# Kernel optimization log

Measured on AMD Instinct MI355X. Metric: run time of the kernel, lower is better.

The kernel has to match this reference:

```python
import jax, jax.numpy as jnp
import numpy as np

B, S, D, H = 2, 2048, 1024, 16
DH = D // H
DIM_K = 1024


def setup_inputs() -> dict:
    key = jax.random.key(0)
    ks = jax.random.split(key, 5)
    sc = 0.02
    return {
        "x": jax.random.normal(ks[0], (B, S, D), dtype=jnp.float32),
        "Wq": jax.random.normal(ks[1], (D, DIM_K), dtype=jnp.float32) * sc,
        "Wk": jax.random.normal(ks[2], (D, DIM_K), dtype=jnp.float32) * sc,
        "Wv": jax.random.normal(ks[3], (D, DIM_K), dtype=jnp.float32) * sc,
        "Wo": jax.random.normal(ks[4], (DIM_K, DIM_K), dtype=jnp.float32) * sc,
    }


def reference(x, Wq, Wk, Wv, Wo):
    # projections (Linear, no bias); weights stored as [in, out]
    q = (x @ Wq).reshape(B, S, H, DH).transpose(0, 2, 1, 3)  # [B,H,S,DH]
    k = (x @ Wk).reshape(B, S, H, DH).transpose(0, 2, 1, 3)
    v = (x @ Wv).reshape(B, S, H, DH).transpose(0, 2, 1, 3)

    scores = jnp.einsum("bhqd,bhkd->bhqk", q, k)  # [B,H,S,S]
    # causal mask applied BEFORE scaling, as in the original
    causal_mask = jnp.triu(jnp.ones((S, S), dtype=bool), k=1)
    m_inf = -jnp.finfo(scores.dtype).max
    scores = jnp.where(causal_mask[None, None], m_inf, scores)
    attn = jax.nn.softmax(scores * (DIM_K ** -0.5), axis=-1)

    out = jnp.einsum("bhqk,bhkd->bhqd", attn, v)  # [B,H,S,DH]
    out = out.transpose(0, 2, 1, 3).reshape(B, S, DIM_K)
    return out @ Wo
```

## Files before the change

kernel.cpp:

```cpp
#include <hip/hip_runtime.h>


#define AS1 __attribute__((address_space(1)))
#define AS3 __attribute__((address_space(3)))
#define EXPC2 0.04508422f
#define C24 1.08202128f

typedef __attribute__((ext_vector_type(4))) float f32x4;
typedef __attribute__((ext_vector_type(8))) short bf16x8;

__device__ __forceinline__ void gload16(const void* g, void* l) {
  __builtin_amdgcn_global_load_lds((const AS1 unsigned int*)g,
                                   (AS3 unsigned int*)l, 16, 0, 0);
}
__device__ __forceinline__ unsigned short f2b(float f) {
  unsigned u = __float_as_uint(f);
  return (unsigned short)((u + 0x7FFFu + ((u >> 16) & 1u)) >> 16);
}
__device__ __forceinline__ float fexp2(float x) {
  float r;
  asm("v_exp_f32 %0, %1" : "=v"(r) : "v"(x));
  return r;
}
__device__ __forceinline__ unsigned cvtpk(float a, float b) {
  unsigned r;
  asm("v_cvt_pk_bf16_f32 %0, %1, %2" : "=v"(r) : "v"(a), "v"(b));
  return r;
}

__global__ __launch_bounds__(256) void prep(
    const float* __restrict__ x, const float* __restrict__ W0,
    const float* __restrict__ W1, const float* __restrict__ W2,
    const float* __restrict__ W3, unsigned short* __restrict__ xb,
    unsigned short* __restrict__ Wt) {
  __shared__ float T[64][65];
  const int tid = threadIdx.x;
  const int bid = blockIdx.x;
  if (bid < 4096) {
    const size_t i = (size_t)(bid * 256 + tid) * 4;
    float4 v = *(const float4*)&x[i];
    uint2 o;
    o.x = f2b(v.x) | ((unsigned)f2b(v.y) << 16);
    o.y = f2b(v.z) | ((unsigned)f2b(v.w) << 16);
    *(uint2*)&xb[i] = o;
    return;
  }
  const int idx = bid - 4096;
  const int kb = (idx & 15) * 64, nb = ((idx >> 4) & 15) * 64, z = idx >> 8;
  const float* W = (z == 0) ? W0 : (z == 1) ? W1 : (z == 2) ? W2 : W3;
  unsigned short* D = Wt + (size_t)z * 1024 * 1024;
#pragma unroll
  for (int p = 0; p < 4; ++p) {
    const int s = p * 256 + tid;
    const int r = s >> 4, c4 = s & 15;
    float4 v = *(const float4*)&W[(size_t)(kb + r) * 1024 + nb + c4 * 4];
    T[r][c4 * 4 + 0] = v.x;
    T[r][c4 * 4 + 1] = v.y;
    T[r][c4 * 4 + 2] = v.z;
    T[r][c4 * 4 + 3] = v.w;
  }
  __syncthreads();
#pragma unroll
  for (int p = 0; p < 4; ++p) {
    const int s = p * 256 + tid;
    const int n = s >> 4, k4 = s & 15;
    uint2 o;
    o.x = f2b(T[k4 * 4 + 0][n]) | ((unsigned)f2b(T[k4 * 4 + 1][n]) << 16);
    o.y = f2b(T[k4 * 4 + 2][n]) | ((unsigned)f2b(T[k4 * 4 + 3][n]) << 16);
    *(uint2*)&D[(size_t)(nb + n) * 1024 + kb + k4 * 4] = o;
  }
}

__global__ __launch_bounds__(256) void gemm_qkv(
    const unsigned short* __restrict__ xb, const unsigned short* __restrict__ Wt,
    unsigned short* __restrict__ Qb, unsigned short* __restrict__ Kb,
    unsigned short* __restrict__ Vp) {
  __shared__ unsigned short smem[32768];

  const int tid = threadIdx.x, lane = tid & 63, w = tid >> 6;
  const int bid = blockIdx.x;
  const int xcd = bid & 7, pos = bid >> 3;
  const int sub = pos >> 5, idx = pos & 31;
  const int bm = xcd * 4 + (idx & 3);
  const int bn = sub * 8 + (idx >> 2);
  const int wr = w >> 1, wc = w & 1;

  f32x4 acc[4][4];
#pragma unroll
  for (int m = 0; m < 4; ++m)
#pragma unroll
    for (int n = 0; n < 4; ++n) acc[m][n] = (f32x4)0.0f;

  const int prow0 = tid >> 3, pc0 = tid & 7;
  const int u0 = pc0 ^ (prow0 & 7);
  const int rOff = 2 * prow0 + (u0 >> 2);
  const int cOff = (u0 & 3) * 8;

  const int fr = lane & 15, g = lane >> 4;
  const int frh = fr >> 1;
  const int pcx = ((((fr & 1) << 2) | g) ^ frh) * 8;

#define QST(BUF, KC)                                                          \
  {                                                                           \
    const size_t ko = (size_t)(KC) + cOff;                                    \
    gload16(&xb[(size_t)(bm * 128 + rOff) * 1024 + ko],                       \
            &smem[(BUF)*8192 + tid * 8]);                                     \
    gload16(&xb[(size_t)(bm * 128 + 64 + rOff) * 1024 + ko],                  \
            &smem[(BUF)*8192 + 2048 + tid * 8]);                              \
    gload16(&Wt[(size_t)(bn * 128 + rOff) * 1024 + ko],                       \
            &smem[(BUF)*8192 + 4096 + tid * 8]);                              \
    gload16(&Wt[(size_t)(bn * 128 + 64 + rOff) * 1024 + ko],                  \
            &smem[(BUF)*8192 + 6144 + tid * 8]);                              \
  }

#define QPH(CB, VMSTR, STAGESTMT)                                             \
  {                                                                           \
    asm volatile(VMSTR ::: "memory");                                         \
    __builtin_amdgcn_sched_barrier(0);                                        \
    __builtin_amdgcn_s_barrier();                                             \
    __builtin_amdgcn_sched_barrier(0);                                        \
    bf16x8 af[4], bf[4];                                                      \
    const unsigned short* Ab_ = &smem[(CB)*8192];                             \
    const unsigned short* Bb_ = &smem[(CB)*8192 + 4096];                      \
    _Pragma("unroll") for (int mf = 0; mf < 4; ++mf) af[mf] =                 \
        *(const bf16x8*)&Ab_[(wr * 32 + mf * 8 + frh) * 64 + pcx];            \
    _Pragma("unroll") for (int nf = 0; nf < 4; ++nf) bf[nf] =                 \
        *(const bf16x8*)&Bb_[(wc * 32 + nf * 8 + frh) * 64 + pcx];            \
    STAGESTMT;                                                                \
    __builtin_amdgcn_s_setprio(1);                                            \
    _Pragma("unroll") for (int mf = 0; mf < 4; ++mf)                          \
        _Pragma("unroll") for (int nf = 0; nf < 4; ++nf) acc[mf][nf] =        \
            __builtin_amdgcn_mfma_f32_16x16x32_bf16(af[mf], bf[nf],           \
                                                    acc[mf][nf], 0, 0, 0);    \
    __builtin_amdgcn_s_setprio(0);                                            \
  }

  QST(0, 0)
  QST(1, 32)
  QST(2, 64)

#pragma unroll 1
  for (int t = 0; t < 29; ++t) {
    const int cb = t & 3, sb = (t + 3) & 3, kc = (t + 3) * 32;
    QPH(cb, "s_waitcnt vmcnt(8)", QST(sb, kc))
  }
  QPH(1, "s_waitcnt vmcnt(8)", (void)0)
  QPH(2, "s_waitcnt vmcnt(4)", (void)0)
  QPH(3, "s_waitcnt vmcnt(0)", (void)0)

  if (bn < 16) {
    unsigned short* Ob = (bn < 8) ? Qb : Kb;
    const int cbase = (bn & 7) * 128;
#pragma unroll
    for (int mf = 0; mf < 4; ++mf)
#pragma unroll
      for (int nf = 0; nf < 4; ++nf) {
        const int col = cbase + wc * 64 + nf * 16 + fr;
        const int h = col >> 6, d = col & 63;
#pragma unroll
        for (int rr = 0; rr < 4; ++rr) {
          const int m = bm * 128 + wr * 64 + mf * 16 + g * 4 + rr;
          const int b = m >> 11, s = m & 2047;
          Ob[((size_t)(b * 16 + h) * 2048 + s) * 64 + d] = f2b(acc[mf][nf][rr]);
        }
      }
    return;
  }

  __syncthreads();
#pragma unroll
  for (int mf = 0; mf < 4; ++mf)
#pragma unroll
    for (int nf = 0; nf < 4; ++nf) {
      const int cl = wc * 64 + nf * 16 + fr;
#pragma unroll
      for (int rr = 0; rr < 4; ++rr) {
        const int ml = wr * 64 + mf * 16 + g * 4 + rr;
        const int u = ml & 63, a = u >> 4;
        const int sperm = (ml & 64) | ((a >> 1) * 32 + ((u >> 2) & 3) * 8 +
                                       (a & 1) * 4 + (u & 3));
        smem[cl * 132 + sperm] = f2b(acc[mf][nf][rr]);
      }
    }
  __syncthreads();
  const int l5 = lane & 31;
  const size_t sbase = (size_t)((bm * 128) & 2047);
  const int bV = bm >> 4;
#pragma unroll
  for (int it = 0; it < 16; ++it) {
    const int rl = w * 32 + it * 2 + (lane >> 5);
    const int rowg = (bn - 16) * 128 + rl;
    const int h = rowg >> 6, d = rowg & 63;
    uint2 v = *(const uint2*)&smem[rl * 132 + l5 * 4];
    *(uint2*)&Vp[((size_t)(bV * 16 + h) * 64 + d) * 2048 + sbase + l5 * 4] = v;
  }
#undef QPH
#undef QST
}

__global__ __launch_bounds__(256) void gemm_out(
    const unsigned short* __restrict__ A, const unsigned short* __restrict__ B,
    float* __restrict__ Of) {
  __shared__ unsigned short smem[32768];

  const int tid = threadIdx.x, lane = tid & 63, w = tid >> 6;
  const int bm = blockIdx.x >> 3, bn = blockIdx.x & 7;
  const int wr = w >> 1, wc = w & 1;

  f32x4 acc[4][4];
#pragma unroll
  for (int m = 0; m < 4; ++m)
#pragma unroll
    for (int n = 0; n < 4; ++n) acc[m][n] = (f32x4)0.0f;

  const int prow0 = tid >> 3, pc0 = tid & 7;
  const int u0 = pc0 ^ (prow0 & 7);
  const int rOff = 2 * prow0 + (u0 >> 2);
  const int cOff = (u0 & 3) * 8;

  const int fr = lane & 15, g = lane >> 4;
  const int frh = fr >> 1;
  const int pcx = ((((fr & 1) << 2) | g) ^ frh) * 8;

#define OSTAGE4(BUF, KS, KC)                                                  \
  {                                                                           \
    const size_t ko = (size_t)(KC) + (KS)*32 + cOff;                          \
    gload16(&A[(size_t)(bm * 128 + rOff) * 1024 + ko],                        \
            &smem[(BUF)*16384 + (KS)*4096 + tid * 8]);                        \
    gload16(&A[(size_t)(bm * 128 + 64 + rOff) * 1024 + ko],                   \
            &smem[(BUF)*16384 + (KS)*4096 + 2048 + tid * 8]);                 \
    gload16(&B[(size_t)(bn * 128 + rOff) * 1024 + ko],                        \
            &smem[(BUF)*16384 + 8192 + (KS)*4096 + tid * 8]);                 \
    gload16(&B[(size_t)(bn * 128 + 64 + rOff) * 1024 + ko],                   \
            &smem[(BUF)*16384 + 8192 + (KS)*4096 + 2048 + tid * 8]);          \
  }

#define OPHASE(CUR, KS, VMSTR, STAGESTMT)                                     \
  {                                                                           \
    asm volatile(VMSTR ::: "memory");                                         \
    __builtin_amdgcn_sched_barrier(0);                                        \
    __builtin_amdgcn_s_barrier();                                             \
    __builtin_amdgcn_sched_barrier(0);                                        \
    bf16x8 af[4], bf[4];                                                      \
    const unsigned short* Ab_ = &smem[(CUR)*16384 + (KS)*4096];               \
    const unsigned short* Bb_ = &smem[(CUR)*16384 + 8192 + (KS)*4096];        \
    _Pragma("unroll") for (int mf = 0; mf < 4; ++mf) af[mf] =                 \
        *(const bf16x8*)&Ab_[(wr * 32 + mf * 8 + frh) * 64 + pcx];            \
    _Pragma("unroll") for (int nf = 0; nf < 4; ++nf) bf[nf] =                 \
        *(const bf16x8*)&Bb_[(wc * 32 + nf * 8 + frh) * 64 + pcx];            \
    STAGESTMT;                                                                \
    __builtin_amdgcn_s_setprio(1);                                            \
    _Pragma("unroll") for (int mf = 0; mf < 4; ++mf)                          \
        _Pragma("unroll") for (int nf = 0; nf < 4; ++nf) acc[mf][nf] =        \
            __builtin_amdgcn_mfma_f32_16x16x32_bf16(af[mf], bf[nf],           \
                                                    acc[mf][nf], 0, 0, 0);    \
    __builtin_amdgcn_s_setprio(0);                                            \
  }

  OSTAGE4(0, 0, 0)
  OSTAGE4(0, 1, 0)

#pragma unroll 1
  for (int t = 0; t < 15; ++t) {
    const int cu_ = t & 1, nb_ = (t + 1) & 1;
    const int kc1 = (t + 1) * 64;
    OPHASE(cu_, 0, "s_waitcnt vmcnt(4)", OSTAGE4(nb_, 0, kc1))
    OPHASE(cu_, 1, "s_waitcnt vmcnt(4)", OSTAGE4(nb_, 1, kc1))
  }
  OPHASE(1, 0, "s_waitcnt vmcnt(4)", (void)0)
  OPHASE(1, 1, "s_waitcnt vmcnt(0)", (void)0)

#pragma unroll
  for (int mf = 0; mf < 4; ++mf)
#pragma unroll
    for (int nf = 0; nf < 4; ++nf) {
      const int col = bn * 128 + wc * 64 + nf * 16 + fr;
#pragma unroll
      for (int rr = 0; rr < 4; ++rr) {
        const int m = bm * 128 + wr * 64 + mf * 16 + g * 4 + rr;
        Of[(size_t)m * 1024 + col] = acc[mf][nf][rr];
      }
    }
#undef OPHASE
#undef OSTAGE4
}

__global__ __launch_bounds__(256) void attn_fm(
    const unsigned short* __restrict__ Qb, const unsigned short* __restrict__ Kb,
    const unsigned short* __restrict__ Vp, unsigned short* __restrict__ Ab) {
  __shared__ unsigned short smem[16384];

  const int tid = threadIdx.x, lane = tid & 63, w = tid >> 6;
  const int lo = lane & 15, hi = lane >> 4;

  const int id = blockIdx.x;
  const int bh = (id & 7) * 4 + ((id >> 3) & 3);
  const int rem = id >> 5;
  const int qtr = rem >> 3;
  const int g = rem & 7;
  const int bq = (qtr == 0)   ? 2 * g
                 : (qtr == 1) ? 2 * g + 1
                 : (qtr == 2) ? 31 - 2 * g
                              : 30 - 2 * g;
  const int qw = bq * 64 + w * 16;
  const size_t base = (size_t)bh * (2048 * 64);

  bf16x8 qf[2];
#pragma unroll
  for (int ks = 0; ks < 2; ++ks)
    qf[ks] =
        *(const bf16x8*)&Qb[base + (size_t)(qw + lo) * 64 + ks * 32 + hi * 8];

  f32x4 accO[4];
#pragma unroll
  for (int mf = 0; mf < 4; ++mf) accO[mf] = (f32x4)0.0f;
  float lpart = 0.0f;

  const int ntile = bq + 1;
  const unsigned short* kgb = Kb + base;
  const unsigned short* vgb = Vp + base;
  const int lseg = w * 512;

#define STAGE(BUF, KBASE)                                                    \
  {                                                                          \
    const int kb_ = (KBASE);                                                 \
    _Pragma("unroll") for (int qq = 0; qq < 2; ++qq) {                       \
      const int slot = qq * 256 + tid;                                       \
      const int row = slot >> 3, ch = (slot & 7) ^ (row & 7);                \
      gload16(kgb + (size_t)(kb_ + row) * 64 + ch * 8,                       \
              &smem[(BUF)*4096 + qq * 2048 + lseg]);                         \
      gload16(vgb + (size_t)row * 2048 + kb_ + ch * 8,                       \
              &smem[8192 + (BUF)*4096 + qq * 2048 + lseg]);                  \
    }                                                                        \
  }

  STAGE(0, 0)
  int cur = 0;

  for (int t = 0; t < ntile; ++t) {
    __syncthreads();
    if (t + 1 < ntile) STAGE(cur ^ 1, (t + 1) * 64)

    const int kb = t * 64;
    const int x7 = lo & 7;
    bf16x8 ka[2][4];
#pragma unroll
    for (int ks = 0; ks < 2; ++ks) {
      const int ch = (ks * 4 + hi) ^ x7;
#pragma unroll
      for (int kf = 0; kf < 4; ++kf)
        ka[ks][kf] =
            *(const bf16x8*)&smem[cur * 4096 + (kf * 16 + lo) * 64 + ch * 8];
    }
    f32x4 st[4];
#pragma unroll
    for (int kf = 0; kf < 4; ++kf) st[kf] = (f32x4)0.0f;
    __builtin_amdgcn_s_setprio(1);
#pragma unroll
    for (int ks = 0; ks < 2; ++ks)
#pragma unroll
      for (int kf = 0; kf < 4; ++kf)
        st[kf] = __builtin_amdgcn_mfma_f32_16x16x32_bf16(ka[ks][kf], qf[ks],
                                                         st[kf], 0, 0, 0);
    __builtin_amdgcn_s_setprio(0);

    bf16x8 va[2][4];
#pragma unroll
    for (int ks = 0; ks < 2; ++ks) {
      const int ch = (ks * 4 + hi) ^ x7;
#pragma unroll
      for (int mf = 0; mf < 4; ++mf)
        va[ks][mf] = *(const bf16x8*)&smem[8192 + cur * 4096 +
                                           (mf * 16 + lo) * 64 + ch * 8];
    }

    float v[16];
#pragma unroll
    for (int kf = 0; kf < 4; ++kf)
#pragma unroll
      for (int rr = 0; rr < 4; ++rr) v[kf * 4 + rr] = st[kf][rr];
    if (kb + 63 > qw) {
      const int qg = qw + lo;
#pragma unroll
      for (int kf = 0; kf < 4; ++kf)
#pragma unroll
        for (int rr = 0; rr < 4; ++rr)
          if (kb + kf * 16 + hi * 4 + rr > qg) v[kf * 4 + rr] = -1e30f;
    }
    float p[16], rs = 0.0f;
#pragma unroll
    for (int i = 0; i < 16; ++i) {
      p[i] = fexp2(fmaf(v[i], EXPC2, -C24));
      rs += p[i];
    }
    lpart += rs;

    bf16x8 pb[2];
#pragma unroll
    for (int ks = 0; ks < 2; ++ks) {
      uint4 u;
      u.x = cvtpk(p[ks * 8 + 0], p[ks * 8 + 1]);
      u.y = cvtpk(p[ks * 8 + 2], p[ks * 8 + 3]);
      u.z = cvtpk(p[ks * 8 + 4], p[ks * 8 + 5]);
      u.w = cvtpk(p[ks * 8 + 6], p[ks * 8 + 7]);
      pb[ks] = *(bf16x8*)&u;
    }

    __builtin_amdgcn_s_setprio(1);
#pragma unroll
    for (int ks = 0; ks < 2; ++ks)
#pragma unroll
      for (int mf = 0; mf < 4; ++mf)
        accO[mf] = __builtin_amdgcn_mfma_f32_16x16x32_bf16(va[ks][mf], pb[ks],
                                                           accO[mf], 0, 0, 0);
    __builtin_amdgcn_s_setprio(0);
    cur ^= 1;
  }

  __syncthreads();

  float l = lpart;
  l += __shfl_xor(l, 16);
  l += __shfl_xor(l, 32);
  const float linv = 1.0f / l;
  unsigned short* ot = &smem[w * 1152];
#pragma unroll
  for (int mf = 0; mf < 4; ++mf) {
    uint2 u;
    u.x = cvtpk(accO[mf][0] * linv, accO[mf][1] * linv);
    u.y = cvtpk(accO[mf][2] * linv, accO[mf][3] * linv);
    *(uint2*)&ot[lo * 72 + mf * 16 + hi * 4] = u;
  }
  const int b = bh >> 4, h = bh & 15;
  const int row = lane >> 2, cg = (lane & 3) * 16;
  uint4 o0 = *(const uint4*)&ot[row * 72 + cg];
  uint4 o1 = *(const uint4*)&ot[row * 72 + cg + 8];
  unsigned short* op = &Ab[(size_t)(b * 2048 + qw + row) * 1024 + h * 64 + cg];
  *(uint4*)op = o0;
  *(uint4*)(op + 8) = o1;
#undef STAGE
}

extern "C" void kernel_launch(void* const* d_in, const int* in_sizes, int n_in,
                              void* d_out, int out_size, void* d_ws,
                              size_t ws_size, hipStream_t stream) {
  (void)in_sizes; (void)n_in; (void)out_size; (void)ws_size;
  const float* x = (const float*)d_in[0];
  const float* Wq = (const float*)d_in[1];
  const float* Wk = (const float*)d_in[2];
  const float* Wv = (const float*)d_in[3];
  const float* Wo = (const float*)d_in[4];
  float* out = (float*)d_out;

  char* ws = (char*)d_ws;
  unsigned short* xb = (unsigned short*)(ws);
  unsigned short* Wt = (unsigned short*)(ws + (8u << 20));
  unsigned short* Qb = (unsigned short*)(ws + (16u << 20));
  unsigned short* Kb = (unsigned short*)(ws + (24u << 20));
  unsigned short* Vp = (unsigned short*)(ws + (32u << 20));
  unsigned short* Ab = (unsigned short*)(ws + (40u << 20));
  unsigned short* Wto = Wt + (size_t)3 * 1024 * 1024;

  prep<<<dim3(5120), 256, 0, stream>>>(x, Wq, Wk, Wv, Wo, xb, Wt);
  gemm_qkv<<<dim3(768), 256, 0, stream>>>(xb, Wt, Qb, Kb, Vp);
  attn_fm<<<dim3(1024), 256, 0, stream>>>(Qb, Kb, Vp, Ab);
  gemm_out<<<dim3(256), 256, 0, stream>>>(Ab, Wto, out);
}
```

Before: 94.57 us.

## Double-buffer LDS fragment reads in QKV GEMM and fold softmax scale into Q

The QKV projection GEMM main loop now reads the next stage's A/B fragments from LDS into a second register set while the current stage's MFMAs run, using finer vmcnt/lgkmcnt waits. This hides LDS read latency behind the MFMAs. Separately, the softmax exponent scale is multiplied into Q at store time and the constant offset is dropped, so attention computes exp2 directly on the scores, removing one FMA per element. Launch bounds request 3 blocks per CU, which caps register use and may cause spills given the doubled fragment registers.

```diff
diff --git a/kernel.cpp b/kernel.cpp
--- a/kernel.cpp
+++ b/kernel.cpp
@@ -4,7 +4,6 @@
 #define AS1 __attribute__((address_space(1)))
 #define AS3 __attribute__((address_space(3)))
 #define EXPC2 0.04508422f
-#define C24 1.08202128f
 
 typedef __attribute__((ext_vector_type(4))) float f32x4;
 typedef __attribute__((ext_vector_type(8))) short bf16x8;
@@ -71,7 +70,7 @@
   }
 }
 
-__global__ __launch_bounds__(256) void gemm_qkv(
+__global__ __launch_bounds__(256, 3) void gemm_qkv(
     const unsigned short* __restrict__ xb, const unsigned short* __restrict__ Wt,
     unsigned short* __restrict__ Qb, unsigned short* __restrict__ Kb,
     unsigned short* __restrict__ Vp) {
@@ -113,43 +112,68 @@
             &smem[(BUF)*8192 + 6144 + tid * 8]);                              \
   }
 
-#define QPH(CB, VMSTR, STAGESTMT)                                             \
+#define RDF(CB, AF, BF)                                                       \
   {                                                                           \
-    asm volatile(VMSTR ::: "memory");                                         \
-    __builtin_amdgcn_sched_barrier(0);                                        \
-    __builtin_amdgcn_s_barrier();                                             \
-    __builtin_amdgcn_sched_barrier(0);                                        \
-    bf16x8 af[4], bf[4];                                                      \
     const unsigned short* Ab_ = &smem[(CB)*8192];                             \
     const unsigned short* Bb_ = &smem[(CB)*8192 + 4096];                      \
-    _Pragma("unroll") for (int mf = 0; mf < 4; ++mf) af[mf] =                 \
+    _Pragma("unroll") for (int mf = 0; mf < 4; ++mf) AF[mf] =                 \
         *(const bf16x8*)&Ab_[(wr * 32 + mf * 8 + frh) * 64 + pcx];            \
-    _Pragma("unroll") for (int nf = 0; nf < 4; ++nf) bf[nf] =                 \
+    _Pragma("unroll") for (int nf = 0; nf < 4; ++nf) BF[nf] =                 \
         *(const bf16x8*)&Bb_[(wc * 32 + nf * 8 + frh) * 64 + pcx];            \
-    STAGESTMT;                                                                \
-    __builtin_amdgcn_s_setprio(1);                                            \
-    _Pragma("unroll") for (int mf = 0; mf < 4; ++mf)                          \
-        _Pragma("unroll") for (int nf = 0; nf < 4; ++nf) acc[mf][nf] =        \
-            __builtin_amdgcn_mfma_f32_16x16x32_bf16(af[mf], bf[nf],           \
-                                                    acc[mf][nf], 0, 0, 0);    \
-    __builtin_amdgcn_s_setprio(0);                                            \
-  }
+  }
+
+#define MM(AF, BF)                                                           \
+  {                                                                          \
+    __builtin_amdgcn_s_setprio(1);                                           \
+    _Pragma("unroll") for (int mf = 0; mf < 4; ++mf)                         \
+        _Pragma("unroll") for (int nf = 0; nf < 4; ++nf) acc[mf][nf] =       \
+            __builtin_amdgcn_mfma_f32_16x16x32_bf16(AF[mf], BF[nf],          \
+                                                    acc[mf][nf], 0, 0, 0);   \
+    __builtin_amdgcn_s_setprio(0);                                           \
+  }
+
+#define BODY(T, ACUR, BCUR, ANXT, BNXT)                                      \
+  {                                                                          \
+    if ((T) < 30) {                                                          \
+      asm volatile("s_waitcnt vmcnt(4)" ::: "memory");                       \
+    } else if ((T) == 30) {                                                  \
+      asm volatile("s_waitcnt vmcnt(0)" ::: "memory");                       \
+    }                                                                        \
+    __builtin_amdgcn_sched_barrier(0);                                       \
+    __builtin_amdgcn_s_barrier();                                            \
+    __builtin_amdgcn_sched_barrier(0);                                       \
+    if ((T) < 31) RDF(((T) + 1) & 3, ANXT, BNXT)                             \
+    if ((T) < 29) QST(((T) + 3) & 3, ((T) + 3) * 32)                         \
+    if ((T) < 31) {                                                          \
+      asm volatile("s_waitcnt lgkmcnt(8)" ::: "memory");                     \
+    } else {                                                                 \
+      asm volatile("s_waitcnt lgkmcnt(0)" ::: "memory");                     \
+    }                                                                        \
+    __builtin_amdgcn_sched_barrier(0);                                       \
+    MM(ACUR, BCUR)                                                           \
+  }
+
+  bf16x8 afA[4], bfA[4], afB[4], bfB[4];
 
   QST(0, 0)
   QST(1, 32)
   QST(2, 64)
+  asm volatile("s_waitcnt vmcnt(8)" ::: "memory");
+  __builtin_amdgcn_sched_barrier(0);
+  __builtin_amdgcn_s_barrier();
+  __builtin_amdgcn_sched_barrier(0);
+  RDF(0, afA, bfA)
 
 #pragma unroll 1
-  for (int t = 0; t < 29; ++t) {
-    const int cb = t & 3, sb = (t + 3) & 3, kc = (t + 3) * 32;
-    QPH(cb, "s_waitcnt vmcnt(8)", QST(sb, kc))
-  }
-  QPH(1, "s_waitcnt vmcnt(8)", (void)0)
-  QPH(2, "s_waitcnt vmcnt(4)", (void)0)
-  QPH(3, "s_waitcnt vmcnt(0)", (void)0)
+  for (int t2 = 0; t2 < 16; ++t2) {
+    const int t = t2 * 2;
+    BODY(t, afA, bfA, afB, bfB)
+    BODY(t + 1, afB, bfB, afA, bfA)
+  }
 
   if (bn < 16) {
     unsigned short* Ob = (bn < 8) ? Qb : Kb;
+    const float qs = (bn < 8) ? EXPC2 : 1.0f;
     const int cbase = (bn & 7) * 128;
 #pragma unroll
     for (int mf = 0; mf < 4; ++mf)
@@ -161,7 +185,8 @@
         for (int rr = 0; rr < 4; ++rr) {
           const int m = bm * 128 + wr * 64 + mf * 16 + g * 4 + rr;
           const int b = m >> 11, s = m & 2047;
-          Ob[((size_t)(b * 16 + h) * 2048 + s) * 64 + d] = f2b(acc[mf][nf][rr]);
+          Ob[((size_t)(b * 16 + h) * 2048 + s) * 64 + d] =
+              f2b(acc[mf][nf][rr] * qs);
         }
       }
     return;
@@ -194,7 +219,9 @@
     uint2 v = *(const uint2*)&smem[rl * 132 + l5 * 4];
     *(uint2*)&Vp[((size_t)(bV * 16 + h) * 64 + d) * 2048 + sbase + l5 * 4] = v;
   }
-#undef QPH
+#undef BODY
+#undef MM
+#undef RDF
 #undef QST
 }
 
@@ -390,7 +417,7 @@
     float p[16], rs = 0.0f;
 #pragma unroll
     for (int i = 0; i < 16; ++i) {
-      p[i] = fexp2(fmaf(v[i], EXPC2, -C24));
+      p[i] = fexp2(v[i]);
       rs += p[i];
     }
     lpart += rs;
```

New measurement: 94.95 us. No clear change (+0.4%).
